# Kernel tuning notes

Measured on AMD Instinct MI355X. Metric: run time of the kernel, lower is better.

Reference implementation:

```python
import jax, jax.numpy as jnp
import numpy as np

NUM_LAYERS = 8
REL_SIZE = 16      # heads per layer
KEY_SIZE = 64
HIDDEN = REL_SIZE * KEY_SIZE  # 1024


def _mass_sincos(node_mass):
    # Sinusoidal embedding of scalar mass -> [B, N, 1, KEY_SIZE]
    half = KEY_SIZE // 2
    inv_freq = jnp.exp(-jnp.log(jnp.float32(10000.0)) * jnp.arange(half, dtype=jnp.float32) / half)
    ang = node_mass[..., None, None] * inv_freq  # [B, N, 1, half]
    return jnp.sin(ang), jnp.cos(ang)


def setup_inputs() -> dict:
    key = jax.random.key(0)
    k1, k2, k3, k4 = jax.random.split(key, 4)
    B, N = 4, 2048
    out_dim = HIDDEN * NUM_LAYERS * 2  # 16384
    node = jax.random.normal(k1, (B, N, HIDDEN), dtype=jnp.float32)
    node_mass = jax.random.uniform(k2, (B, N), dtype=jnp.float32) * 100.0
    W = jax.random.normal(k3, (HIDDEN, out_dim), dtype=jnp.float32) * (1.0 / np.sqrt(HIDDEN))
    b = jax.random.normal(k4, (out_dim,), dtype=jnp.float32) * 0.02
    return {"node": node, "node_mass": node_mass, "W": W, "b": b}


def reference(node, node_mass, W, b):
    B, N, _ = node.shape
    H = REL_SIZE * NUM_LAYERS  # heads per cache (k or v)
    # Fused KV projection: [B, N, 2*H, KEY_SIZE]
    kv = (jnp.einsum('bnh,ho->bno', node, W) + b).reshape(B, N, 2 * H, KEY_SIZE)
    k_cache, v_cache = kv[:, :, :H, :], kv[:, :, H:, :]
    # Rotary-style rotation of k_cache by mass sin/cos (broadcast over heads)
    dis_sin, dis_cos = _mass_sincos(node_mass)      # each [B, N, 1, KEY_SIZE//2]
    half = KEY_SIZE // 2
    x0, x1 = k_cache[..., :half], k_cache[..., half:]
    k_cache = jnp.concatenate([x0 * dis_cos - x1 * dis_sin,
                               x0 * dis_sin + x1 * dis_cos], axis=-1)
    # transpose(1, 2): [B, H, N, KEY_SIZE]; per-layer chunks are contiguous slices
    k_out = jnp.swapaxes(k_cache, 1, 2)
    v_out = jnp.swapaxes(v_cache, 1, 2)
    # Stack K and V caches; layer chunks = slices of size REL_SIZE along head dim
    return jnp.stack([k_out, v_out], axis=0)  # [2, B, H, N, KEY_SIZE]
```

## Files before the change

### kernel.cpp

```cpp
#include <hip/hip_runtime.h>
#include <stdint.h>

#define M_TOT 8192
#define N_TOT 16384
#define K_TOT 1024

typedef __bf16 bf16x8 __attribute__((ext_vector_type(8)));
typedef float f32x4 __attribute__((ext_vector_type(4)));

__device__ __forceinline__ unsigned short f2bf(float f) {
  unsigned int u = __float_as_uint(f);
  u = u + 0x7FFFu + ((u >> 16) & 1u);
  return (unsigned short)(u >> 16);
}

__device__ __forceinline__ void gload_lds16(const void* g, void* l) {
  __builtin_amdgcn_global_load_lds(
      (const __attribute__((address_space(1))) unsigned int*)g,
      (__attribute__((address_space(3))) unsigned int*)l,
      16, 0, 0);
}

__global__ __launch_bounds__(256) void k_convert_node(
    const float* __restrict__ src, unsigned short* __restrict__ dst) {
  size_t base = ((size_t)blockIdx.x * 256 + threadIdx.x) * 8;
#pragma unroll
  for (int it = 0; it < 4; it++) {
    size_t i = base + (size_t)it * (1024 * 256 * 8);
    float4 v0 = *(const float4*)(src + i);
    float4 v1 = *(const float4*)(src + i + 4);
    union { unsigned short u[8]; uint4 q; } r;
    r.u[0] = f2bf(v0.x); r.u[1] = f2bf(v0.y); r.u[2] = f2bf(v0.z); r.u[3] = f2bf(v0.w);
    r.u[4] = f2bf(v1.x); r.u[5] = f2bf(v1.y); r.u[6] = f2bf(v1.z); r.u[7] = f2bf(v1.w);
    *(uint4*)(dst + i) = r.q;
  }
}

__global__ __launch_bounds__(256) void k_transpose_w(
    const float* __restrict__ W, unsigned short* __restrict__ Wt) {
  __shared__ float tile[64][65];
  int o0 = blockIdx.x * 64;
  int k0 = blockIdx.y * 64;
  int t = threadIdx.x;
  int kr0 = t >> 4, c4 = t & 15;
#pragma unroll
  for (int i = 0; i < 4; i++) {
    int kr = kr0 + i * 16;
    float4 v = *(const float4*)&W[(size_t)(k0 + kr) * N_TOT + o0 + c4 * 4];
    tile[kr][c4 * 4 + 0] = v.x;
    tile[kr][c4 * 4 + 1] = v.y;
    tile[kr][c4 * 4 + 2] = v.z;
    tile[kr][c4 * 4 + 3] = v.w;
  }
  __syncthreads();
  int or0 = t >> 3, c8 = t & 7;
#pragma unroll
  for (int i = 0; i < 2; i++) {
    int orr = or0 + i * 32;
    union { unsigned short u[8]; uint4 q; } r;
#pragma unroll
    for (int j = 0; j < 8; j++) r.u[j] = f2bf(tile[c8 * 8 + j][orr]);
    *(uint4*)&Wt[(size_t)(o0 + orr) * K_TOT + k0 + c8 * 8] = r.q;
  }
}

__global__ __launch_bounds__(256) void k_sincos(
    const float* __restrict__ mass, float* __restrict__ sin_t, float* __restrict__ cos_t) {
  int t = blockIdx.x * 256 + threadIdx.x;
  int row = t >> 5;
  int d = t & 31;
  float m = mass[row];
  float invf = expf(-0.28782313662425575f * (float)d);
  float ang = m * invf;
  float s, c;
  sincosf(ang, &s, &c);
  sin_t[t] = s;
  cos_t[t] = c;
}

__global__ __launch_bounds__(256, 2) void k_gemm256b(
    const unsigned short* __restrict__ A,
    const unsigned short* __restrict__ Bt,
    const float* __restrict__ bias,
    const float* __restrict__ sin_t,
    const float* __restrict__ cos_t,
    float* __restrict__ out)
{
  extern __shared__ char smem[];

  int tid  = threadIdx.x;
  int lane = tid & 63;
  int wid  = tid >> 6;
  int wm   = wid >> 1;
  int wn   = wid & 1;

  int orig = blockIdx.x;
  int wg = (orig & 7) * 512 + (orig >> 3);
  int bn0 = (wg & 127) * 128;
  int bm0 = (wg >> 7) * 256;

  const unsigned short* srcA = A  + (size_t)(bm0 + (tid >> 2)) * K_TOT + (tid & 3) * 8;
  const unsigned short* srcB = Bt + (size_t)(bn0 + (tid >> 2)) * K_TOT + (tid & 3) * 8;
  const size_t rs64 = (size_t)64 * K_TOT;

  int wofs = wid * 1024;

#define STAGE_A(s_, bo_) do { char* dA = smem + (bo_) + wofs; \
    const unsigned short* sa = srcA + (size_t)(s_) * 32; \
    gload_lds16(sa,            dA); \
    gload_lds16(sa + rs64,     dA + 4096); \
    gload_lds16(sa + 2 * rs64, dA + 8192); \
    gload_lds16(sa + 3 * rs64, dA + 12288); } while (0)
#define STAGE_B(s_, bo_) do { char* dB = smem + (bo_) + 16384 + wofs; \
    const unsigned short* sb = srcB + (size_t)(s_) * 32; \
    gload_lds16(sb,        dB); \
    gload_lds16(sb + rs64, dB + 4096); } while (0)

  STAGE_A(0, 0); STAGE_B(0, 0);
  STAGE_A(1, 24576); STAGE_B(1, 24576);

  f32x4 acc[8][4] = {};

  int r = lane & 15;
  int q = lane >> 4;
  int aoff = (wm * 128 + r) * 64 + q * 16;
  int boff = (wn * 64  + r) * 64 + q * 16;

  int cur = 0;
  int stg = 49152;

  for (int s = 0; s < 32; ++s) {
    if (s < 31) { asm volatile("s_waitcnt vmcnt(6)" ::: "memory"); }
    else        { asm volatile("s_waitcnt vmcnt(0)" ::: "memory"); }
    __builtin_amdgcn_s_barrier();
    __builtin_amdgcn_sched_barrier(0);

    const char* As_ = smem + cur;
    const char* Bs_ = As_ + 16384;

    bf16x8 bfrag[4], afrag[4];
#pragma unroll
    for (int ni = 0; ni < 4; ni++) bfrag[ni] = *(const bf16x8*)(Bs_ + boff + ni * 1024);
#pragma unroll
    for (int mi = 0; mi < 4; mi++) afrag[mi] = *(const bf16x8*)(As_ + aoff + mi * 1024);
    if (s < 30) STAGE_A(s + 2, stg);
    __builtin_amdgcn_s_setprio(1);
#pragma unroll
    for (int mi = 0; mi < 4; mi++)
#pragma unroll
      for (int ni = 0; ni < 4; ni++)
        acc[mi][ni] = __builtin_amdgcn_mfma_f32_16x16x32_bf16(afrag[mi], bfrag[ni], acc[mi][ni], 0, 0, 0);
    __builtin_amdgcn_s_setprio(0);

    bf16x8 afrag2[4];
#pragma unroll
    for (int mi = 0; mi < 4; mi++) afrag2[mi] = *(const bf16x8*)(As_ + aoff + (mi + 4) * 1024);
    if (s < 30) STAGE_B(s + 2, stg);
    __builtin_amdgcn_s_setprio(1);
#pragma unroll
    for (int mi = 0; mi < 4; mi++)
#pragma unroll
      for (int ni = 0; ni < 4; ni++)
        acc[mi + 4][ni] = __builtin_amdgcn_mfma_f32_16x16x32_bf16(afrag2[mi], bfrag[ni], acc[mi + 4][ni], 0, 0, 0);
    __builtin_amdgcn_s_setprio(0);

    stg = cur;
    cur = (cur == 49152) ? 0 : cur + 24576;
  }
#undef STAGE_A
#undef STAGE_B

  int col16 = r;
  float bv[4];
#pragma unroll
  for (int ni = 0; ni < 4; ni++) bv[ni] = bias[bn0 + wn * 64 + ni * 16 + col16];

  int cgrp = (bn0 >> 6) + wn;
  int is_k = (cgrp < 128);
  int h = cgrp & 127;
  size_t sec = is_k ? 0 : 4;

#pragma unroll
  for (int mi = 0; mi < 8; mi++) {
#pragma unroll
    for (int reg = 0; reg < 4; reg++) {
      int row = bm0 + wm * 128 + mi * 16 + q * 4 + reg;
      int bb = row >> 11;
      int n  = row & 2047;
      float* op = out + (((sec + bb) * 128 + h) * 2048 + (size_t)n) * 64;
      if (is_k) {
#pragma unroll
        for (int ni = 0; ni < 2; ni++) {
          int d = ni * 16 + col16;
          float x0 = acc[mi][ni][reg]     + bv[ni];
          float x1 = acc[mi][ni + 2][reg] + bv[ni + 2];
          float sv = sin_t[row * 32 + d];
          float cv = cos_t[row * 32 + d];
          op[d]      = x0 * cv - x1 * sv;
          op[d + 32] = x0 * sv + x1 * cv;
        }
      } else {
#pragma unroll
        for (int ni = 0; ni < 4; ni++) {
          int d = ni * 16 + col16;
          op[d] = acc[mi][ni][reg] + bv[ni];
        }
      }
    }
  }
}

extern "C" void kernel_launch(void* const* d_in, const int* in_sizes, int n_in,
                              void* d_out, int out_size, void* d_ws, size_t ws_size,
                              hipStream_t stream) {
  const float* node = (const float*)d_in[0];
  const float* mass = (const float*)d_in[1];
  const float* W    = (const float*)d_in[2];
  const float* bias = (const float*)d_in[3];
  float* out = (float*)d_out;

  const size_t NODE_B  = (size_t)M_TOT * K_TOT * 2;
  const size_t WT_B    = (size_t)N_TOT * K_TOT * 2;
  const size_t SIN_B   = (size_t)M_TOT * 32 * 4;
  if (ws_size < NODE_B + WT_B + 2 * SIN_B) return;

  char* ws = (char*)d_ws;
  unsigned short* nodeB = (unsigned short*)ws;
  unsigned short* WtB   = (unsigned short*)(ws + NODE_B);
  float* sin_t = (float*)(ws + NODE_B + WT_B);
  float* cos_t = (float*)(ws + NODE_B + WT_B + SIN_B);

  (void)hipFuncSetAttribute((const void*)k_gemm256b,
                            hipFuncAttributeMaxDynamicSharedMemorySize, 73728);

  k_convert_node<<<1024, 256, 0, stream>>>(node, nodeB);
  k_transpose_w<<<dim3(N_TOT / 64, K_TOT / 64), 256, 0, stream>>>(W, WtB);
  k_sincos<<<(M_TOT * 32) / 256, 256, 0, stream>>>(mass, sin_t, cos_t);
  k_gemm256b<<<dim3((M_TOT / 256) * (N_TOT / 128)), dim3(256), 73728, stream>>>(
      nodeB, WtB, bias, sin_t, cos_t, out);
}
```

Baseline: 382.4 us.

## Rewrite GEMM as 256x256 tile, 8-wave block with swizzled LDS and 8-phase pipeline

The projection GEMM moves from a 256x128 tile with 4 waves to a 256x256 tile with 8 waves per block, using a BK=64 double buffer of 128 KB LDS. LDS layouts are XOR-swizzled to avoid bank conflicts, and the main loop is split into four phases per K step. Each phase interleaves the next global-to-LDS loads, fragment reads and MFMA bursts between barriers. Blocks are remapped so neighbouring groups share A and B tiles in L2, giving more data reuse per load at the cost of one block per CU and more barriers.

```diff
diff --git a/kernel.cpp b/kernel.cpp
--- a/kernel.cpp
+++ b/kernel.cpp
@@ -78,7 +78,7 @@
   cos_t[t] = c;
 }
 
-__global__ __launch_bounds__(256, 2) void k_gemm256b(
+__global__ __launch_bounds__(512, 1) void k_gemm256c(
     const unsigned short* __restrict__ A,
     const unsigned short* __restrict__ Bt,
     const float* __restrict__ bias,
@@ -91,84 +91,111 @@
   int tid  = threadIdx.x;
   int lane = tid & 63;
   int wid  = tid >> 6;
-  int wm   = wid >> 1;
-  int wn   = wid & 1;
+  int wm   = wid >> 2;
+  int wn   = wid & 3;
 
   int orig = blockIdx.x;
-  int wg = (orig & 7) * 512 + (orig >> 3);
-  int bn0 = (wg & 127) * 128;
-  int bm0 = (wg >> 7) * 256;
-
-  const unsigned short* srcA = A  + (size_t)(bm0 + (tid >> 2)) * K_TOT + (tid & 3) * 8;
-  const unsigned short* srcB = Bt + (size_t)(bn0 + (tid >> 2)) * K_TOT + (tid & 3) * 8;
-  const size_t rs64 = (size_t)64 * K_TOT;
+  int x  = orig & 7;
+  int cc = orig >> 3;
+  int st = cc >> 4;
+  int w  = cc & 15;
+  int bm0 = (x * 4 + (w >> 2)) * 256;
+  int bn0 = (st * 4 + (w & 3)) * 256;
+
+  int rowA = tid >> 3;
+  int sA   = (tid & 7) ^ (rowA & 7);
+  const unsigned short* gA = A + (size_t)(bm0 + rowA) * K_TOT + sA * 8;
+  int rowB = tid >> 2;
+  int qB   = (tid & 3) ^ (rowB & 3);
+  const unsigned short* gB = Bt + (size_t)(bn0 + rowB) * K_TOT + qB * 8;
 
   int wofs = wid * 1024;
 
-#define STAGE_A(s_, bo_) do { char* dA = smem + (bo_) + wofs; \
-    const unsigned short* sa = srcA + (size_t)(s_) * 32; \
-    gload_lds16(sa,            dA); \
-    gload_lds16(sa + rs64,     dA + 4096); \
-    gload_lds16(sa + 2 * rs64, dA + 8192); \
-    gload_lds16(sa + 3 * rs64, dA + 12288); } while (0)
-#define STAGE_B(s_, bo_) do { char* dB = smem + (bo_) + 16384 + wofs; \
-    const unsigned short* sb = srcB + (size_t)(s_) * 32; \
-    gload_lds16(sb,        dB); \
-    gload_lds16(sb + rs64, dB + 4096); } while (0)
-
-  STAGE_A(0, 0); STAGE_B(0, 0);
-  STAGE_A(1, 24576); STAGE_B(1, 24576);
+#define STG_A(t_, mq) do { \
+    char* d_ = smem + ((t_) & 1) * 65536 + (mq) * 16384 + wofs;            \
+    const unsigned short* s_ = gA + (size_t)((mq) * 64) * K_TOT + (t_) * 64; \
+    gload_lds16(s_, d_);                                                     \
+    gload_lds16(s_ + (size_t)128 * K_TOT, d_ + 8192); } while (0)
+#define STG_B(t_, kh) do { \
+    char* d_ = smem + ((t_) & 1) * 65536 + 32768 + (kh) * 16384 + wofs;    \
+    const unsigned short* s_ = gB + (t_) * 64 + (kh) * 32;                   \
+    gload_lds16(s_, d_);                                                     \
+    gload_lds16(s_ + (size_t)128 * K_TOT, d_ + 8192); } while (0)
 
   f32x4 acc[8][4] = {};
+  bf16x8 bK[4], aF[4];
 
   int r = lane & 15;
   int q = lane >> 4;
-  int aoff = (wm * 128 + r) * 64 + q * 16;
-  int boff = (wn * 64  + r) * 64 + q * 16;
-
-  int cur = 0;
-  int stg = 49152;
-
-  for (int s = 0; s < 32; ++s) {
-    if (s < 31) { asm volatile("s_waitcnt vmcnt(6)" ::: "memory"); }
-    else        { asm volatile("s_waitcnt vmcnt(0)" ::: "memory"); }
-    __builtin_amdgcn_s_barrier();
-    __builtin_amdgcn_sched_barrier(0);
-
-    const char* As_ = smem + cur;
-    const char* Bs_ = As_ + 16384;
-
-    bf16x8 bfrag[4], afrag[4];
-#pragma unroll
-    for (int ni = 0; ni < 4; ni++) bfrag[ni] = *(const bf16x8*)(Bs_ + boff + ni * 1024);
-#pragma unroll
-    for (int mi = 0; mi < 4; mi++) afrag[mi] = *(const bf16x8*)(As_ + aoff + mi * 1024);
-    if (s < 30) STAGE_A(s + 2, stg);
-    __builtin_amdgcn_s_setprio(1);
-#pragma unroll
-    for (int mi = 0; mi < 4; mi++)
-#pragma unroll
-      for (int ni = 0; ni < 4; ni++)
-        acc[mi][ni] = __builtin_amdgcn_mfma_f32_16x16x32_bf16(afrag[mi], bfrag[ni], acc[mi][ni], 0, 0, 0);
-    __builtin_amdgcn_s_setprio(0);
-
-    bf16x8 afrag2[4];
-#pragma unroll
-    for (int mi = 0; mi < 4; mi++) afrag2[mi] = *(const bf16x8*)(As_ + aoff + (mi + 4) * 1024);
-    if (s < 30) STAGE_B(s + 2, stg);
-    __builtin_amdgcn_s_setprio(1);
-#pragma unroll
-    for (int mi = 0; mi < 4; mi++)
-#pragma unroll
-      for (int ni = 0; ni < 4; ni++)
-        acc[mi + 4][ni] = __builtin_amdgcn_mfma_f32_16x16x32_bf16(afrag2[mi], bfrag[ni], acc[mi + 4][ni], 0, 0, 0);
-    __builtin_amdgcn_s_setprio(0);
-
-    stg = cur;
-    cur = (cur == 49152) ? 0 : cur + 24576;
-  }
-#undef STAGE_A
-#undef STAGE_B
+  int aOff = (wm * 64 + r) * 128;
+  int ks0  = ((q)     ^ (r & 7)) * 16;
+  int ks1  = ((4 + q) ^ (r & 7)) * 16;
+  int bOff = 32768 + (wn * 64 + r) * 64 + ((q ^ (r & 3)) * 16);
+
+#define RD_B(db_, kh) { _Pragma("unroll") \
+    for (int ni = 0; ni < 4; ni++) \
+      bK[ni] = *(const bf16x8*)((db_) + bOff + (kh) * 16384 + ni * 1024); }
+#define RD_A(db_, mq, ks_) { _Pragma("unroll") \
+    for (int i = 0; i < 4; i++) \
+      aF[i] = *(const bf16x8*)((db_) + (mq) * 16384 + aOff + i * 2048 + (ks_)); }
+#define MF_LO { _Pragma("unroll") for (int mi = 0; mi < 4; mi++) \
+    _Pragma("unroll") for (int ni = 0; ni < 4; ni++) \
+      acc[mi][ni] = __builtin_amdgcn_mfma_f32_16x16x32_bf16(aF[mi], bK[ni], acc[mi][ni], 0, 0, 0); }
+#define MF_HI { _Pragma("unroll") for (int mi = 0; mi < 4; mi++) \
+    _Pragma("unroll") for (int ni = 0; ni < 4; ni++) \
+      acc[mi + 4][ni] = __builtin_amdgcn_mfma_f32_16x16x32_bf16(aF[mi], bK[ni], acc[mi + 4][ni], 0, 0, 0); }
+
+#define W8 asm volatile("s_waitcnt vmcnt(8)" ::: "memory")
+#define W4 asm volatile("s_waitcnt vmcnt(4)" ::: "memory")
+#define W2 asm volatile("s_waitcnt vmcnt(2)" ::: "memory")
+#define W0 asm volatile("s_waitcnt vmcnt(0)" ::: "memory")
+#define BAR1 do { __builtin_amdgcn_s_barrier(); \
+    asm volatile("s_waitcnt lgkmcnt(0)" ::: "memory"); \
+    __builtin_amdgcn_sched_barrier(0); \
+    __builtin_amdgcn_s_setprio(1); } while (0)
+#define BAR2 do { __builtin_amdgcn_s_setprio(0); \
+    __builtin_amdgcn_s_barrier(); \
+    __builtin_amdgcn_sched_barrier(0); } while (0)
+
+  STG_B(0, 0); STG_A(0, 0); STG_A(0, 1); STG_B(0, 1);
+  STG_B(1, 0); STG_A(1, 0);
+  W8;
+  __builtin_amdgcn_s_barrier();
+  __builtin_amdgcn_sched_barrier(0);
+
+  for (int t = 0; t < 14; t++) {
+    const char* db = smem + (t & 1) * 65536;
+    STG_A(t + 1, 1); RD_B(db, 0); RD_A(db, 0, ks0); W8; BAR1; MF_LO; BAR2;
+    STG_B(t + 1, 1); RD_A(db, 1, ks0);              W8; BAR1; MF_HI; BAR2;
+    STG_B(t + 2, 0); RD_B(db, 1); RD_A(db, 0, ks1); W8; BAR1; MF_LO; BAR2;
+    STG_A(t + 2, 0); RD_A(db, 1, ks1);              W8; BAR1; MF_HI; BAR2;
+  }
+  {
+    const char* db = smem;
+    STG_A(15, 1); RD_B(db, 0); RD_A(db, 0, ks0); W8; BAR1; MF_LO; BAR2;
+    STG_B(15, 1); RD_A(db, 1, ks0);              W8; BAR1; MF_HI; BAR2;
+                  RD_B(db, 1); RD_A(db, 0, ks1); W8; BAR1; MF_LO; BAR2;
+                  RD_A(db, 1, ks1);              W4; BAR1; MF_HI; BAR2;
+  }
+  {
+    const char* db = smem + 65536;
+    RD_B(db, 0); RD_A(db, 0, ks0); W2; BAR1; MF_LO; BAR2;
+    RD_A(db, 1, ks0);              W0; BAR1; MF_HI; BAR2;
+    RD_B(db, 1); RD_A(db, 0, ks1);     BAR1; MF_LO; BAR2;
+    RD_A(db, 1, ks1);                  BAR1; MF_HI; BAR2;
+  }
+#undef STG_A
+#undef STG_B
+#undef RD_B
+#undef RD_A
+#undef MF_LO
+#undef MF_HI
+#undef W8
+#undef W4
+#undef W2
+#undef W0
+#undef BAR1
+#undef BAR2
 
   int col16 = r;
   float bv[4];
@@ -194,10 +221,10 @@
           int d = ni * 16 + col16;
           float x0 = acc[mi][ni][reg]     + bv[ni];
           float x1 = acc[mi][ni + 2][reg] + bv[ni + 2];
-          float sv = sin_t[row * 32 + d];
-          float cv = cos_t[row * 32 + d];
-          op[d]      = x0 * cv - x1 * sv;
-          op[d + 32] = x0 * sv + x1 * cv;
+          float sv2 = sin_t[row * 32 + d];
+          float cv2 = cos_t[row * 32 + d];
+          op[d]      = x0 * cv2 - x1 * sv2;
+          op[d + 32] = x0 * sv2 + x1 * cv2;
         }
       } else {
 #pragma unroll
@@ -230,12 +257,12 @@
   float* sin_t = (float*)(ws + NODE_B + WT_B);
   float* cos_t = (float*)(ws + NODE_B + WT_B + SIN_B);
 
-  (void)hipFuncSetAttribute((const void*)k_gemm256b,
-                            hipFuncAttributeMaxDynamicSharedMemorySize, 73728);
+  (void)hipFuncSetAttribute((const void*)k_gemm256c,
+                            hipFuncAttributeMaxDynamicSharedMemorySize, 131072);
 
   k_convert_node<<<1024, 256, 0, stream>>>(node, nodeB);
   k_transpose_w<<<dim3(N_TOT / 64, K_TOT / 64), 256, 0, stream>>>(W, WtB);
   k_sincos<<<(M_TOT * 32) / 256, 256, 0, stream>>>(mass, sin_t, cos_t);
-  k_gemm256b<<<dim3((M_TOT / 256) * (N_TOT / 128)), dim3(256), 73728, stream>>>(
+  k_gemm256c<<<dim3((M_TOT / 256) * (N_TOT / 256)), dim3(512), 131072, stream>>>(
       nodeB, WtB, bias, sin_t, cos_t, out);
 }
```

Measured after the change: 360.9 us. -5.6%, faster.
